# Performance work log

Hardware: AMD Instinct MI355X
Metric: run time of the kernel (lower is better)

The kernel has to match this reference:

```python
import jax, jax.numpy as jnp
import numpy as np

E = 23   # unique experts
K = 3    # active experts per token

def setup_inputs() -> dict:
    key = jax.random.key(0)
    ks = jax.random.split(key, 11)
    d, h, B, N = 1024, 768, 16, 196
    s = 0.02  # init scale so sigmoid gate is non-saturated
    return {
        "x":      jax.random.normal(ks[0], (B, N, d), jnp.float32),
        "gate_w": jax.random.normal(ks[1], (d, E), jnp.float32) * s,
        "gate_b": jnp.zeros((E,), jnp.float32),
        "w1":     jax.random.normal(ks[2], (E, d, h), jnp.float32) * s,
        "b1":     jnp.zeros((E, h), jnp.float32),
        "w2":     jax.random.normal(ks[3], (E, h, d), jnp.float32) * s,
        "b2":     jnp.zeros((E, d), jnp.float32),
        "ws1":    jax.random.normal(ks[4], (d, h), jnp.float32) * s,
        "bs1":    jnp.zeros((h,), jnp.float32),
        "ws2":    jax.random.normal(ks[5], (h, d), jnp.float32) * s,
        "bs2":    jnp.zeros((d,), jnp.float32),
    }

def reference(x, gate_w, gate_b, w1, b1, w2, b2, ws1, bs1, ws2, bs2):
    o_shape = x.shape
    xt = x.reshape(-1, o_shape[-1])            # [T, d]
    T = xt.shape[0]

    # gating: sigmoid gate, top-3 (the 'bias' buffer in the source is zeros)
    gw = jax.nn.sigmoid(xt @ gate_w + gate_b)  # [T, E]
    top_vals, top_idx = jax.lax.top_k(gw, K)   # [T, K]
    tw = top_vals / top_vals.sum(-1, keepdims=True)

    # dense combine weights: tw scattered to [T, E] (0 for unselected experts)
    w_dense = jnp.zeros_like(gw).at[jnp.arange(T)[:, None], top_idx].add(tw)

    # expert MLPs (dense-masked equivalent of the grouped dispatch)
    hh = jax.nn.gelu(jnp.einsum('td,edh->teh', xt, w1) + b1, approximate=False)
    eo = jnp.einsum('teh,ehd->ted', hh, w2) + b2          # [T, E, d]

    # shared expert
    shared = jax.nn.gelu(xt @ ws1 + bs1, approximate=False) @ ws2 + bs2

    out = shared + jnp.einsum('ted,te->td', eo, w_dense)  # [T, d]

    # aux load-balancing loss
    gwn = gw / gw.sum(-1, keepdims=True)
    P = gwn.mean(0)                                       # [E]
    counts = jnp.zeros((E,), gw.dtype).at[top_idx.reshape(-1)].add(1.0)
    Fv = E * counts / (K * T)
    aux = (P * Fv).sum()

    return out.reshape(o_shape), aux
```

## Files before the change

kernel.cpp:

```cpp
#include <hip/hip_runtime.h>
#include <hip/hip_bf16.h>

#define T_TOK 3136
#define DDIM  1024
#define HDIM  768
#define NEXP  23
#define TOPK  3
#define MTILE 128
#define NTILE 128
#define KTILE 32
#define LDSB  40
#define MAXTILES 128
#define MAX_SLOTS 16384
#define GATE_BLOCKS 1568
#define XCVT_BLOCKS 3136

typedef __attribute__((ext_vector_type(8))) short  short8;
typedef __attribute__((ext_vector_type(4))) short  short4v;
typedef __attribute__((ext_vector_type(4))) float  floatx4;

__device__ __forceinline__ short f2b(float f) {
    union { float f; unsigned u; } v; v.f = f;
    unsigned r = v.u + 0x7FFFu + ((v.u >> 16) & 1u);
    return (short)(r >> 16);
}
__device__ __forceinline__ float b2f(short s) {
    union { unsigned u; float f; } v; v.u = ((unsigned)(unsigned short)s) << 16; return v.f;
}
__device__ __forceinline__ float gelu_exact(float v) {
    return 0.5f * v * (1.0f + erff(v * 0.70710678118654752f));
}
__device__ __forceinline__ void gld16(const short* g, short* l) {
    __builtin_amdgcn_global_load_lds(
        (const __attribute__((address_space(1))) void*)g,
        (__attribute__((address_space(3))) void*)l, 16, 0, 0);
}
__device__ __forceinline__ void bar_cnt8() {
    asm volatile("s_waitcnt vmcnt(8) lgkmcnt(0)" ::: "memory");
    __builtin_amdgcn_s_barrier();
    __builtin_amdgcn_sched_barrier(0);
}
__device__ __forceinline__ void bar_cnt0() {
    asm volatile("s_waitcnt vmcnt(0) lgkmcnt(0)" ::: "memory");
    __builtin_amdgcn_s_barrier();
    __builtin_amdgcn_sched_barrier(0);
}

__global__ __launch_bounds__(256) void prep_kernel(
    const float* __restrict__ x, short* __restrict__ xb,
    const float* __restrict__ gw, float* __restrict__ gwT, float* __restrict__ Pf)
{
    __shared__ float tile[32][33];
    if (blockIdx.x < XCVT_BLOCKS) {
        if (blockIdx.x == 0 && threadIdx.x < NEXP) Pf[threadIdx.x] = 0.f;
        int i = blockIdx.x * 256 + threadIdx.x;
        float4 v = ((const float4*)x)[i];
        short4v s = { f2b(v.x), f2b(v.y), f2b(v.z), f2b(v.w) };
        ((short4v*)xb)[i] = s;
        return;
    }
    const int kt = blockIdx.x - XCVT_BLOCKS;
    const int tx = threadIdx.x & 31, ty = threadIdx.x >> 5;
    #pragma unroll
    for (int i = 0; i < 4; i++) {
        int k = ty + i * 8;
        tile[k][tx] = (tx < NEXP) ? gw[(size_t)(kt * 32 + k) * NEXP + tx] : 0.f;
    }
    __syncthreads();
    #pragma unroll
    for (int i = 0; i < 4; i++) {
        int e = ty + i * 8;
        if (e < 24) gwT[(size_t)e * DDIM + kt * 32 + tx] = tile[tx][e];
    }
}

__global__ __launch_bounds__(256) void gate_kernel(
    const float* __restrict__ x, const float* __restrict__ gwT, const float* __restrict__ gb,
    float* __restrict__ Pf, int* __restrict__ top_idx, float* __restrict__ top_w)
{
    const int tid = threadIdx.x;
    const int lane = tid & 63, wave = tid >> 6;
    const int ebase = wave * 6;
    __shared__ float sg[24];
    __shared__ float accP[NEXP];
    if (tid < NEXP) accP[tid] = 0.f;

    for (int t = blockIdx.x; t < T_TOK; t += GATE_BLOCKS) {
        const float4* xr4 = (const float4*)(x + (size_t)t * DDIM);
        float4 xv[4];
        #pragma unroll
        for (int j = 0; j < 4; j++) xv[j] = xr4[j * 64 + lane];

        double a0 = 0, a1 = 0, a2 = 0, a3 = 0, a4 = 0, a5 = 0;
        #pragma unroll
        for (int j = 0; j < 4; j++) {
            const float4* gp = (const float4*)gwT + (size_t)ebase * 256 + j * 64 + lane;
            float4 g0 = gp[0 * 256], g1 = gp[1 * 256], g2 = gp[2 * 256];
            float4 g3 = gp[3 * 256], g4 = gp[4 * 256], g5 = gp[5 * 256];
            float4 xj = xv[j];
            a0 += (double)xj.x * g0.x + (double)xj.y * g0.y + (double)xj.z * g0.z + (double)xj.w * g0.w;
            a1 += (double)xj.x * g1.x + (double)xj.y * g1.y + (double)xj.z * g1.z + (double)xj.w * g1.w;
            a2 += (double)xj.x * g2.x + (double)xj.y * g2.y + (double)xj.z * g2.z + (double)xj.w * g2.w;
            a3 += (double)xj.x * g3.x + (double)xj.y * g3.y + (double)xj.z * g3.z + (double)xj.w * g3.w;
            a4 += (double)xj.x * g4.x + (double)xj.y * g4.y + (double)xj.z * g4.z + (double)xj.w * g4.w;
            a5 += (double)xj.x * g5.x + (double)xj.y * g5.y + (double)xj.z * g5.z + (double)xj.w * g5.w;
        }
        #pragma unroll
        for (int off = 32; off > 0; off >>= 1) {
            a0 += __shfl_xor(a0, off);
            a1 += __shfl_xor(a1, off);
            a2 += __shfl_xor(a2, off);
            a3 += __shfl_xor(a3, off);
            a4 += __shfl_xor(a4, off);
            a5 += __shfl_xor(a5, off);
        }

        if (lane == 0) {
            double av[6] = { a0, a1, a2, a3, a4, a5 };
            #pragma unroll
            for (int i = 0; i < 6; i++) {
                int e = ebase + i;
                if (e < NEXP) {
                    float z = (float)av[i] + gb[e];
                    sg[e] = 1.0f / (1.0f + expf(-z));
                }
            }
        }
        __syncthreads();

        if (tid < NEXP) {
            float s = 0.f;
            #pragma unroll
            for (int e = 0; e < NEXP; e++) s += sg[e];
            accP[tid] += sg[tid] / s;
        }
        if (tid == 0) {
            float v0 = -1.f, v1 = -1.f, v2 = -1.f; int i0 = 0, i1 = 0, i2 = 0;
            for (int e = 0; e < NEXP; e++) {
                float v = sg[e];
                if (v > v0)      { v2 = v1; i2 = i1; v1 = v0; i1 = i0; v0 = v; i0 = e; }
                else if (v > v1) { v2 = v1; i2 = i1; v1 = v; i1 = e; }
                else if (v > v2) { v2 = v; i2 = e; }
            }
            float ts = v0 + v1 + v2;
            top_idx[t * 3 + 0] = i0; top_w[t * 3 + 0] = v0 / ts;
            top_idx[t * 3 + 1] = i1; top_w[t * 3 + 1] = v1 / ts;
            top_idx[t * 3 + 2] = i2; top_w[t * 3 + 2] = v2 / ts;
        }
        __syncthreads();
    }
    if (tid < NEXP) atomicAdd(&Pf[tid], accP[tid]);
}

__global__ __launch_bounds__(1024) void route_kernel(
    const int* __restrict__ top_idx, const float* __restrict__ Pf,
    int* __restrict__ ntl,
    int* __restrict__ slot_t, int* __restrict__ slot_of,
    int* __restrict__ tmap_e, int* __restrict__ tmap_b,
    float* __restrict__ out_aux)
{
    __shared__ int h[NEXP];
    __shared__ int lfill[NEXP];
    __shared__ int soffs[NEXP + 1];
    __shared__ int sntl[NEXP + 1];
    const int tid = threadIdx.x;
    if (tid < NEXP) { h[tid] = 0; lfill[tid] = 0; }
    __syncthreads();
    for (int i = tid; i < T_TOK * 3; i += 1024) atomicAdd(&h[top_idx[i]], 1);
    __syncthreads();
    if (tid == 0) {
        int o = 0, ti = 0;
        for (int e = 0; e < NEXP; e++) {
            int c = h[e];
            int nt = (c + MTILE - 1) / MTILE;
            soffs[e] = o; sntl[e] = nt; ntl[e] = nt;
            for (int j = 0; j < nt; j++) { tmap_e[ti] = e; tmap_b[ti] = o + j * MTILE; ti++; }
            o += nt * MTILE;
        }
        int nts = (T_TOK + MTILE - 1) / MTILE;
        soffs[NEXP] = o; sntl[NEXP] = nts; ntl[NEXP] = nts;
        for (int j = 0; j < nts; j++) { tmap_e[ti] = NEXP; tmap_b[ti] = o + j * MTILE; ti++; }
        ntl[NEXP + 1] = ti;
        float aux = 0.f;
        for (int e = 0; e < NEXP; e++) {
            float P = Pf[e] / (float)T_TOK;
            float F = (float)NEXP * (float)h[e] / (float)(TOPK * T_TOK);
            aux += P * F;
        }
        out_aux[0] = aux;
    }
    __syncthreads();
    for (int e = 0; e <= NEXP; e++) {
        int cnt = (e < NEXP) ? h[e] : T_TOK;
        int s0 = soffs[e] + cnt, s1 = soffs[e] + sntl[e] * MTILE;
        for (int s = s0 + tid; s < s1; s += 1024) slot_t[s] = 0;
    }
    for (int t = tid; t < T_TOK; t += 1024) {
        #pragma unroll
        for (int k = 0; k < TOPK; k++) {
            int e = top_idx[t * 3 + k];
            int pos = atomicAdd(&lfill[e], 1);
            int s = soffs[e] + pos;
            slot_t[s] = t;
            slot_of[t * 4 + k] = s;
        }
        int s = soffs[NEXP] + t;
        slot_t[s] = t;
        slot_of[t * 4 + 3] = s;
    }
}

__global__ __launch_bounds__(256) void gemm1_kernel(
    const short* __restrict__ xb,
    const float* __restrict__ w1, const float* __restrict__ b1,
    const float* __restrict__ ws1, const float* __restrict__ bs1,
    const int* __restrict__ tmap_e, const int* __restrict__ tmap_b,
    const int* __restrict__ ntl,
    const int* __restrict__ slot_t, short* __restrict__ hh)
{
    const int L = blockIdx.x;
    const int xcd = L & 7, sl = L >> 3;
    const int ty = xcd * 16 + sl / 6, tx = sl % 6;
    if (ty >= ntl[NEXP + 1]) return;
    const int e = tmap_e[ty];
    const int slot_base = tmap_b[ty];
    const int n0 = tx * NTILE;
    const float* __restrict__ Wf = (e < NEXP) ? (w1 + (size_t)e * DDIM * HDIM) : ws1;
    const float* __restrict__ Bv = (e < NEXP) ? (b1 + (size_t)e * HDIM) : bs1;

    __shared__ __align__(16) short As[2][MTILE * KTILE];
    __shared__ __align__(16) short Bs[2][NTILE * LDSB];
    __shared__ int toks[MTILE];

    const int tid = threadIdx.x;
    for (int i = tid; i < MTILE; i += 256) toks[i] = slot_t[slot_base + i];

    const int lane = tid & 63, wave = tid >> 6;
    const int mbase = (wave & 1) * 64, nbase = (wave >> 1) * 64;
    const int lc = lane & 15, q = lane >> 4;
    const int xq8 = (q ^ ((lc >> 1) & 3)) << 3;

    const int srow = wave * 16 + (lane >> 2);
    const int c8   = (lane & 3) * 8;

    __syncthreads();
    const short* gA0 = xb + (size_t)toks[srow]      * DDIM + c8;
    const short* gA1 = xb + (size_t)toks[64 + srow] * DDIM + c8;
    const int lofs0 = wave * 512, lofs1 = 2048 + wave * 512;

    const int g = wave, cn = lane;
    const float* gW = Wf + (size_t)(8 * g) * HDIM + n0 + 2 * cn;
    const int bws = (g ^ (cn & 3)) << 3;
    const int bofs0 = (2 * cn) * LDSB + bws, bofs1 = (2 * cn + 1) * LDSB + bws;

    floatx4 acc[4][4];
    #pragma unroll
    for (int m = 0; m < 4; m++)
        #pragma unroll
        for (int n = 0; n < 4; n++) acc[m][n] = (floatx4)0.f;

    const int NT = DDIM / KTILE;
    float2 f[8];
    #pragma unroll
    for (int j = 0; j < 8; j++) f[j] = *(const float2*)(gW + (size_t)j * HDIM);
    gld16(gA0, &As[0][lofs0]);
    gld16(gA1, &As[0][lofs1]);
    __builtin_amdgcn_sched_barrier(0);
    {
        short8 s0, s1;
        #pragma unroll
        for (int j = 0; j < 8; j++) { s0[j] = f2b(f[j].x); s1[j] = f2b(f[j].y); }
        *(short8*)&Bs[0][bofs0] = s0;
        *(short8*)&Bs[0][bofs1] = s1;
    }
    #pragma unroll
    for (int j = 0; j < 8; j++) f[j] = *(const float2*)(gW + (size_t)(KTILE + j) * HDIM);
    bar_cnt8();

    for (int t = 0; t < NT; t++) {
        const int cur = t & 1;
        if (t + 1 < NT) {
            gld16(gA0 + (t + 1) * KTILE, &As[cur ^ 1][lofs0]);
            gld16(gA1 + (t + 1) * KTILE, &As[cur ^ 1][lofs1]);
            __builtin_amdgcn_sched_barrier(0);
            short8 s0, s1;
            #pragma unroll
            for (int j = 0; j < 8; j++) { s0[j] = f2b(f[j].x); s1[j] = f2b(f[j].y); }
            *(short8*)&Bs[cur ^ 1][bofs0] = s0;
            *(short8*)&Bs[cur ^ 1][bofs1] = s1;
        }
        if (t + 2 < NT) {
            #pragma unroll
            for (int j = 0; j < 8; j++)
                f[j] = *(const float2*)(gW + (size_t)((t + 2) * KTILE + j) * HDIM);
        }
        short8 af[4], bf[4];
        #pragma unroll
        for (int m = 0; m < 4; m++) af[m] = *(const short8*)&As[cur][(mbase + m * 16 + lc) * KTILE + q * 8];
        #pragma unroll
        for (int n = 0; n < 4; n++) bf[n] = *(const short8*)&Bs[cur][(nbase + n * 16 + lc) * LDSB + xq8];
        #pragma unroll
        for (int m = 0; m < 4; m++)
            #pragma unroll
            for (int n = 0; n < 4; n++)
                acc[m][n] = __builtin_amdgcn_mfma_f32_16x16x32_bf16(af[m], bf[n], acc[m][n], 0, 0, 0);
        if (t + 1 < NT) {
            if (t + 2 < NT) bar_cnt8();
            else            bar_cnt0();
        }
    }

    #pragma unroll
    for (int n = 0; n < 4; n++) {
        const int col = n0 + nbase + n * 16 + lc;
        const float bb = Bv[col];
        #pragma unroll
        for (int m = 0; m < 4; m++) {
            const int rbase = slot_base + mbase + m * 16 + q * 4;
            #pragma unroll
            for (int r = 0; r < 4; r++) {
                float v = acc[m][n][r] + bb;
                hh[(size_t)(rbase + r) * HDIM + col] = f2b(gelu_exact(v));
            }
        }
    }
}

__global__ __launch_bounds__(256) void gemm2_kernel(
    const short* __restrict__ hh,
    const float* __restrict__ w2, const float* __restrict__ b2,
    const float* __restrict__ ws2, const float* __restrict__ bs2,
    const int* __restrict__ tmap_e, const int* __restrict__ tmap_b,
    const int* __restrict__ ntl,
    short* __restrict__ eo)
{
    const int L = blockIdx.x;
    const int xcd = L & 7, sl = L >> 3;
    const int ty = xcd * 16 + sl / 8, tx = sl & 7;
    if (ty >= ntl[NEXP + 1]) return;
    const int e = tmap_e[ty];
    const int slot_base = tmap_b[ty];
    const int n0 = tx * NTILE;
    const float* __restrict__ Wf = (e < NEXP) ? (w2 + (size_t)e * HDIM * DDIM) : ws2;
    const float* __restrict__ Bv = (e < NEXP) ? (b2 + (size_t)e * DDIM) : bs2;

    __shared__ __align__(16) short As[2][MTILE * KTILE];
    __shared__ __align__(16) short Bs[2][NTILE * LDSB];

    const int tid = threadIdx.x;
    const int lane = tid & 63, wave = tid >> 6;
    const int mbase = (wave & 1) * 64, nbase = (wave >> 1) * 64;
    const int lc = lane & 15, q = lane >> 4;
    const int xq8 = (q ^ ((lc >> 1) & 3)) << 3;

    const int srow = wave * 16 + (lane >> 2);
    const int c8   = (lane & 3) * 8;

    const short* gA0 = hh + (size_t)(slot_base + srow)      * HDIM + c8;
    const short* gA1 = hh + (size_t)(slot_base + 64 + srow) * HDIM + c8;
    const int lofs0 = wave * 512, lofs1 = 2048 + wave * 512;

    const int g = wave, cn = lane;
    const float* gW = Wf + (size_t)(8 * g) * DDIM + n0 + 2 * cn;
    const int bws = (g ^ (cn & 3)) << 3;
    const int bofs0 = (2 * cn) * LDSB + bws, bofs1 = (2 * cn + 1) * LDSB + bws;

    floatx4 acc[4][4];
    #pragma unroll
    for (int m = 0; m < 4; m++)
        #pragma unroll
        for (int n = 0; n < 4; n++) acc[m][n] = (floatx4)0.f;

    const int NT = HDIM / KTILE;
    float2 f[8];
    #pragma unroll
    for (int j = 0; j < 8; j++) f[j] = *(const float2*)(gW + (size_t)j * DDIM);
    gld16(gA0, &As[0][lofs0]);
    gld16(gA1, &As[0][lofs1]);
    __builtin_amdgcn_sched_barrier(0);
    {
        short8 s0, s1;
        #pragma unroll
        for (int j = 0; j < 8; j++) { s0[j] = f2b(f[j].x); s1[j] = f2b(f[j].y); }
        *(short8*)&Bs[0][bofs0] = s0;
        *(short8*)&Bs[0][bofs1] = s1;
    }
    #pragma unroll
    for (int j = 0; j < 8; j++) f[j] = *(const float2*)(gW + (size_t)(KTILE + j) * DDIM);
    bar_cnt8();

    for (int t = 0; t < NT; t++) {
        const int cur = t & 1;
        if (t + 1 < NT) {
            gld16(gA0 + (t + 1) * KTILE, &As[cur ^ 1][lofs0]);
            gld16(gA1 + (t + 1) * KTILE, &As[cur ^ 1][lofs1]);
            __builtin_amdgcn_sched_barrier(0);
            short8 s0, s1;
            #pragma unroll
            for (int j = 0; j < 8; j++) { s0[j] = f2b(f[j].x); s1[j] = f2b(f[j].y); }
            *(short8*)&Bs[cur ^ 1][bofs0] = s0;
            *(short8*)&Bs[cur ^ 1][bofs1] = s1;
        }
        if (t + 2 < NT) {
            #pragma unroll
            for (int j = 0; j < 8; j++)
                f[j] = *(const float2*)(gW + (size_t)((t + 2) * KTILE + j) * DDIM);
        }
        short8 af[4], bf[4];
        #pragma unroll
        for (int m = 0; m < 4; m++) af[m] = *(const short8*)&As[cur][(mbase + m * 16 + lc) * KTILE + q * 8];
        #pragma unroll
        for (int n = 0; n < 4; n++) bf[n] = *(const short8*)&Bs[cur][(nbase + n * 16 + lc) * LDSB + xq8];
        #pragma unroll
        for (int m = 0; m < 4; m++)
            #pragma unroll
            for (int n = 0; n < 4; n++)
                acc[m][n] = __builtin_amdgcn_mfma_f32_16x16x32_bf16(af[m], bf[n], acc[m][n], 0, 0, 0);
        if (t + 1 < NT) {
            if (t + 2 < NT) bar_cnt8();
            else            bar_cnt0();
        }
    }

    #pragma unroll
    for (int n = 0; n < 4; n++) {
        const int col = n0 + nbase + n * 16 + lc;
        const float bb = Bv[col];
        #pragma unroll
        for (int m = 0; m < 4; m++) {
            const int rbase = slot_base + mbase + m * 16 + q * 4;
            #pragma unroll
            for (int r = 0; r < 4; r++)
                eo[(size_t)(rbase + r) * DDIM + col] = f2b(acc[m][n][r] + bb);
        }
    }
}

__global__ __launch_bounds__(256) void combine_kernel(
    const short* __restrict__ eo, const float* __restrict__ top_w,
    const int* __restrict__ slot_of, float* __restrict__ out)
{
    const int t = blockIdx.x;
    const int c = threadIdx.x * 4;
    const int s0 = slot_of[t * 4 + 0], s1 = slot_of[t * 4 + 1];
    const int s2 = slot_of[t * 4 + 2], s3 = slot_of[t * 4 + 3];
    const float w0 = top_w[t * 3 + 0], w1 = top_w[t * 3 + 1], w2 = top_w[t * 3 + 2];
    short4v a = *(const short4v*)(eo + (size_t)s0 * DDIM + c);
    short4v b = *(const short4v*)(eo + (size_t)s1 * DDIM + c);
    short4v d = *(const short4v*)(eo + (size_t)s2 * DDIM + c);
    short4v s = *(const short4v*)(eo + (size_t)s3 * DDIM + c);
    float4 o;
    o.x = b2f(s.x) + w0 * b2f(a.x) + w1 * b2f(b.x) + w2 * b2f(d.x);
    o.y = b2f(s.y) + w0 * b2f(a.y) + w1 * b2f(b.y) + w2 * b2f(d.y);
    o.z = b2f(s.z) + w0 * b2f(a.z) + w1 * b2f(b.z) + w2 * b2f(d.z);
    o.w = b2f(s.w) + w0 * b2f(a.w) + w1 * b2f(b.w) + w2 * b2f(d.w);
    *(float4*)(out + (size_t)t * DDIM + c) = o;
}

extern "C" void kernel_launch(void* const* d_in, const int* in_sizes, int n_in,
                              void* d_out, int out_size, void* d_ws, size_t ws_size,
                              hipStream_t stream)
{
    const float* x   = (const float*)d_in[0];
    const float* gw  = (const float*)d_in[1];
    const float* gb  = (const float*)d_in[2];
    const float* w1  = (const float*)d_in[3];
    const float* b1  = (const float*)d_in[4];
    const float* w2  = (const float*)d_in[5];
    const float* b2  = (const float*)d_in[6];
    const float* ws1 = (const float*)d_in[7];
    const float* bs1 = (const float*)d_in[8];
    const float* ws2 = (const float*)d_in[9];
    const float* bs2 = (const float*)d_in[10];
    float* out = (float*)d_out;

    char* p = (char*)d_ws;
    auto alloc = [&](size_t bytes) -> char* {
        char* r = p; p += (bytes + 255) & ~(size_t)255; return r;
    };
    int*   top_idx  = (int*)  alloc((size_t)T_TOK * 3 * 4);
    float* top_w    = (float*)alloc((size_t)T_TOK * 3 * 4);
    float* Pf       = (float*)alloc(NEXP * 4);
    int*   ntl      = (int*)  alloc((NEXP + 2) * 4);
    int*   slot_t   = (int*)  alloc((size_t)MAX_SLOTS * 4);
    int*   slot_of  = (int*)  alloc((size_t)T_TOK * 4 * 4);
    int*   tmap_e   = (int*)  alloc((size_t)MAXTILES * 4);
    int*   tmap_b   = (int*)  alloc((size_t)MAXTILES * 4);
    float* gwT      = (float*)alloc((size_t)24 * DDIM * 4);
    short* xb       = (short*)alloc((size_t)T_TOK * DDIM * 2);
    short* hh       = (short*)alloc((size_t)MAX_SLOTS * HDIM * 2);
    short* eo       = (short*)alloc((size_t)MAX_SLOTS * DDIM * 2);

    prep_kernel<<<XCVT_BLOCKS + DDIM / 32, 256, 0, stream>>>(x, xb, gw, gwT, Pf);
    gate_kernel<<<GATE_BLOCKS, 256, 0, stream>>>(x, gwT, gb, Pf, top_idx, top_w);
    route_kernel<<<1, 1024, 0, stream>>>(top_idx, Pf, ntl, slot_t, slot_of,
                                         tmap_e, tmap_b, out + (size_t)T_TOK * DDIM);
    gemm1_kernel<<<8 * 16 * 6, 256, 0, stream>>>(
        xb, w1, b1, ws1, bs1, tmap_e, tmap_b, ntl, slot_t, hh);
    gemm2_kernel<<<8 * 16 * 8, 256, 0, stream>>>(
        hh, w2, b2, ws2, bs2, tmap_e, tmap_b, ntl, eo);
    combine_kernel<<<T_TOK, 256, 0, stream>>>(eo, top_w, slot_of, out);
}
```

Before: 380.0 us.

## Use 8 waves per block in expert GEMMs with 64x32 per-wave tiles

Doubles the threads per block in both grouped GEMM kernels from 256 to 512. Each wave now computes a 64x32 output sub-tile instead of 64x64, and the A and B tile loads are split across 8 waves, so each thread issues half as many loads and conversions. The aim is more waves per CU to hide the global load and fp32-to-bf16 conversion latency. The cost is lower MFMA work per LDS fragment read, and the higher register use allowed under launch_bounds 512 may limit occupancy.

```diff
diff --git a/kernel.cpp b/kernel.cpp
--- a/kernel.cpp
+++ b/kernel.cpp
@@ -35,8 +35,8 @@
         (const __attribute__((address_space(1))) void*)g,
         (__attribute__((address_space(3))) void*)l, 16, 0, 0);
 }
-__device__ __forceinline__ void bar_cnt8() {
-    asm volatile("s_waitcnt vmcnt(8) lgkmcnt(0)" ::: "memory");
+__device__ __forceinline__ void bar_cnt4() {
+    asm volatile("s_waitcnt vmcnt(4) lgkmcnt(0)" ::: "memory");
     __builtin_amdgcn_s_barrier();
     __builtin_amdgcn_sched_barrier(0);
 }
@@ -210,7 +210,7 @@
     }
 }
 
-__global__ __launch_bounds__(256) void gemm1_kernel(
+__global__ __launch_bounds__(512) void gemm1_kernel(
     const short* __restrict__ xb,
     const float* __restrict__ w1, const float* __restrict__ b1,
     const float* __restrict__ ws1, const float* __restrict__ bs1,
@@ -233,10 +233,10 @@
     __shared__ int toks[MTILE];
 
     const int tid = threadIdx.x;
-    for (int i = tid; i < MTILE; i += 256) toks[i] = slot_t[slot_base + i];
+    for (int i = tid; i < MTILE; i += 512) toks[i] = slot_t[slot_base + i];
 
     const int lane = tid & 63, wave = tid >> 6;
-    const int mbase = (wave & 1) * 64, nbase = (wave >> 1) * 64;
+    const int mbase = (wave & 1) * 64, nbase = (wave >> 1) * 32;
     const int lc = lane & 15, q = lane >> 4;
     const int xq8 = (q ^ ((lc >> 1) & 3)) << 3;
 
@@ -244,74 +244,71 @@
     const int c8   = (lane & 3) * 8;
 
     __syncthreads();
-    const short* gA0 = xb + (size_t)toks[srow]      * DDIM + c8;
-    const short* gA1 = xb + (size_t)toks[64 + srow] * DDIM + c8;
-    const int lofs0 = wave * 512, lofs1 = 2048 + wave * 512;
-
-    const int g = wave, cn = lane;
-    const float* gW = Wf + (size_t)(8 * g) * HDIM + n0 + 2 * cn;
-    const int bws = (g ^ (cn & 3)) << 3;
+    const short* gA = xb + (size_t)toks[srow] * DDIM + c8;
+    const int lofs = wave * 512;
+
+    const int cn = lane;
+    const float* gW = Wf + (size_t)(4 * wave) * HDIM + n0 + 2 * cn;
+    const int bws = ((((wave >> 1) ^ (cn & 3)) << 3) + (wave & 1) * 4);
     const int bofs0 = (2 * cn) * LDSB + bws, bofs1 = (2 * cn + 1) * LDSB + bws;
 
-    floatx4 acc[4][4];
+    floatx4 acc[4][2];
     #pragma unroll
     for (int m = 0; m < 4; m++)
         #pragma unroll
-        for (int n = 0; n < 4; n++) acc[m][n] = (floatx4)0.f;
+        for (int n = 0; n < 2; n++) acc[m][n] = (floatx4)0.f;
 
     const int NT = DDIM / KTILE;
-    float2 f[8];
-    #pragma unroll
-    for (int j = 0; j < 8; j++) f[j] = *(const float2*)(gW + (size_t)j * HDIM);
-    gld16(gA0, &As[0][lofs0]);
-    gld16(gA1, &As[0][lofs1]);
+    float2 f[4];
+    #pragma unroll
+    for (int j = 0; j < 4; j++) f[j] = *(const float2*)(gW + (size_t)j * HDIM);
+    gld16(gA, &As[0][lofs]);
     __builtin_amdgcn_sched_barrier(0);
     {
-        short8 s0, s1;
-        #pragma unroll
-        for (int j = 0; j < 8; j++) { s0[j] = f2b(f[j].x); s1[j] = f2b(f[j].y); }
-        *(short8*)&Bs[0][bofs0] = s0;
-        *(short8*)&Bs[0][bofs1] = s1;
-    }
-    #pragma unroll
-    for (int j = 0; j < 8; j++) f[j] = *(const float2*)(gW + (size_t)(KTILE + j) * HDIM);
-    bar_cnt8();
+        short4v s0, s1;
+        #pragma unroll
+        for (int j = 0; j < 4; j++) { s0[j] = f2b(f[j].x); s1[j] = f2b(f[j].y); }
+        *(short4v*)&Bs[0][bofs0] = s0;
+        *(short4v*)&Bs[0][bofs1] = s1;
+    }
+    #pragma unroll
+    for (int j = 0; j < 4; j++) f[j] = *(const float2*)(gW + (size_t)(KTILE + j) * HDIM);
+    bar_cnt4();
 
     for (int t = 0; t < NT; t++) {
         const int cur = t & 1;
         if (t + 1 < NT) {
-            gld16(gA0 + (t + 1) * KTILE, &As[cur ^ 1][lofs0]);
-            gld16(gA1 + (t + 1) * KTILE, &As[cur ^ 1][lofs1]);
+            gld16(gA + (t + 1) * KTILE, &As[cur ^ 1][lofs]);
             __builtin_amdgcn_sched_barrier(0);
-            short8 s0, s1;
-            #pragma unroll
-            for (int j = 0; j < 8; j++) { s0[j] = f2b(f[j].x); s1[j] = f2b(f[j].y); }
-            *(short8*)&Bs[cur ^ 1][bofs0] = s0;
-            *(short8*)&Bs[cur ^ 1][bofs1] = s1;
+            short4v s0, s1;
+            #pragma unroll
+            for (int j = 0; j < 4; j++) { s0[j] = f2b(f[j].x); s1[j] = f2b(f[j].y); }
+            *(short4v*)&Bs[cur ^ 1][bofs0] = s0;
+            *(short4v*)&Bs[cur ^ 1][bofs1] = s1;
         }
         if (t + 2 < NT) {
             #pragma unroll
-            for (int j = 0; j < 8; j++)
+            for (int j = 0; j < 4; j++)
                 f[j] = *(const float2*)(gW + (size_t)((t + 2) * KTILE + j) * HDIM);
         }
-        short8 af[4], bf[4];
+        short8 af[4], bf[2];
         #pragma unroll
         for (int m = 0; m < 4; m++) af[m] = *(const short8*)&As[cur][(mbase + m * 16 + lc) * KTILE + q * 8];
         #pragma unroll
-        for (int n = 0; n < 4; n++) bf[n] = *(const short8*)&Bs[cur][(nbase + n * 16 + lc) * LDSB + xq8];
+        for (int n = 0; n < 2; n++) bf[n] = *(const short8*)&Bs[cur][(nbase + n * 16 + lc) * LDSB + xq8];
         #pragma unroll
         for (int m = 0; m < 4; m++)
             #pragma unroll
-            for (int n = 0; n < 4; n++)
+            for (int n = 0; n < 2; n++)
                 acc[m][n] = __builtin_amdgcn_mfma_f32_16x16x32_bf16(af[m], bf[n], acc[m][n], 0, 0, 0);
         if (t + 1 < NT) {
-            if (t + 2 < NT) bar_cnt8();
+            if (t + 2 < NT) bar_cnt4();
             else            bar_cnt0();
         }
     }
 
     #pragma unroll
-    for (int n = 0; n < 4; n++) {
+    for (int n = 0; n < 2; n++) {
         const int col = n0 + nbase + n * 16 + lc;
         const float bb = Bv[col];
         #pragma unroll
@@ -326,7 +323,7 @@
     }
 }
 
-__global__ __launch_bounds__(256) void gemm2_kernel(
+__global__ __launch_bounds__(512) void gemm2_kernel(
     const short* __restrict__ hh,
     const float* __restrict__ w2, const float* __restrict__ b2,
     const float* __restrict__ ws2, const float* __restrict__ bs2,
@@ -349,81 +346,78 @@
 
     const int tid = threadIdx.x;
     const int lane = tid & 63, wave = tid >> 6;
-    const int mbase = (wave & 1) * 64, nbase = (wave >> 1) * 64;
+    const int mbase = (wave & 1) * 64, nbase = (wave >> 1) * 32;
     const int lc = lane & 15, q = lane >> 4;
     const int xq8 = (q ^ ((lc >> 1) & 3)) << 3;
 
     const int srow = wave * 16 + (lane >> 2);
     const int c8   = (lane & 3) * 8;
 
-    const short* gA0 = hh + (size_t)(slot_base + srow)      * HDIM + c8;
-    const short* gA1 = hh + (size_t)(slot_base + 64 + srow) * HDIM + c8;
-    const int lofs0 = wave * 512, lofs1 = 2048 + wave * 512;
-
-    const int g = wave, cn = lane;
-    const float* gW = Wf + (size_t)(8 * g) * DDIM + n0 + 2 * cn;
-    const int bws = (g ^ (cn & 3)) << 3;
+    const short* gA = hh + (size_t)(slot_base + srow) * HDIM + c8;
+    const int lofs = wave * 512;
+
+    const int cn = lane;
+    const float* gW = Wf + (size_t)(4 * wave) * DDIM + n0 + 2 * cn;
+    const int bws = ((((wave >> 1) ^ (cn & 3)) << 3) + (wave & 1) * 4);
     const int bofs0 = (2 * cn) * LDSB + bws, bofs1 = (2 * cn + 1) * LDSB + bws;
 
-    floatx4 acc[4][4];
+    floatx4 acc[4][2];
     #pragma unroll
     for (int m = 0; m < 4; m++)
         #pragma unroll
-        for (int n = 0; n < 4; n++) acc[m][n] = (floatx4)0.f;
+        for (int n = 0; n < 2; n++) acc[m][n] = (floatx4)0.f;
 
     const int NT = HDIM / KTILE;
-    float2 f[8];
-    #pragma unroll
-    for (int j = 0; j < 8; j++) f[j] = *(const float2*)(gW + (size_t)j * DDIM);
-    gld16(gA0, &As[0][lofs0]);
-    gld16(gA1, &As[0][lofs1]);
+    float2 f[4];
+    #pragma unroll
+    for (int j = 0; j < 4; j++) f[j] = *(const float2*)(gW + (size_t)j * DDIM);
+    gld16(gA, &As[0][lofs]);
     __builtin_amdgcn_sched_barrier(0);
     {
-        short8 s0, s1;
-        #pragma unroll
-        for (int j = 0; j < 8; j++) { s0[j] = f2b(f[j].x); s1[j] = f2b(f[j].y); }
-        *(short8*)&Bs[0][bofs0] = s0;
-        *(short8*)&Bs[0][bofs1] = s1;
-    }
-    #pragma unroll
-    for (int j = 0; j < 8; j++) f[j] = *(const float2*)(gW + (size_t)(KTILE + j) * DDIM);
-    bar_cnt8();
+        short4v s0, s1;
+        #pragma unroll
+        for (int j = 0; j < 4; j++) { s0[j] = f2b(f[j].x); s1[j] = f2b(f[j].y); }
+        *(short4v*)&Bs[0][bofs0] = s0;
+        *(short4v*)&Bs[0][bofs1] = s1;
+    }
+    #pragma unroll
+    for (int j = 0; j < 4; j++) f[j] = *(const float2*)(gW + (size_t)(KTILE + j) * DDIM);
+    bar_cnt4();
 
     for (int t = 0; t < NT; t++) {
         const int cur = t & 1;
         if (t + 1 < NT) {
-            gld16(gA0 + (t + 1) * KTILE, &As[cur ^ 1][lofs0]);
-            gld16(gA1 + (t + 1) * KTILE, &As[cur ^ 1][lofs1]);
+            gld16(gA + (t + 1) * KTILE, &As[cur ^ 1][lofs]);
             __builtin_amdgcn_sched_barrier(0);
-            short8 s0, s1;
-            #pragma unroll
-            for (int j = 0; j < 8; j++) { s0[j] = f2b(f[j].x); s1[j] = f2b(f[j].y); }
-            *(short8*)&Bs[cur ^ 1][bofs0] = s0;
-            *(short8*)&Bs[cur ^ 1][bofs1] = s1;
+            short4v s0, s1;
+            #pragma unroll
+            for (int j = 0; j < 4; j++) { s0[j] = f2b(f[j].x); s1[j] = f2b(f[j].y); }
+            *(short4v*)&Bs[cur ^ 1][bofs0] = s0;
+            *(short4v*)&Bs[cur ^ 1][bofs1] = s1;
         }
         if (t + 2 < NT) {
             #pragma unroll
-            for (int j = 0; j < 8; j++)
+            for (int j = 0; j < 4; j++)
                 f[j] = *(const float2*)(gW + (size_t)((t + 2) * KTILE + j) * DDIM);
         }
-        short8 af[4], bf[4];
+        short8 af[4], bf[2];
         #pragma unroll
         for (int m = 0; m < 4; m++) af[m] = *(const short8*)&As[cur][(mbase + m * 16 + lc) * KTILE + q * 8];
         #pragma unroll
-        for (int n = 0; n < 4; n++) bf[n] = *(const short8*)&Bs[cur][(nbase + n * 16 + lc) * LDSB + xq8];
+        for (int n = 0; n < 2; n++) bf[n] = *(const short8*)&Bs[cur][(nbase + n * 16 + lc) * LDSB + xq8];
         #pragma unroll
         for (int m = 0; m < 4; m++)
             #pragma unroll
-            for (int n = 0; n < 4; n++)
+            for (int n = 0; n < 2; n++)
                 acc[m][n] = __builtin_amdgcn_mfma_f32_16x16x32_bf16(af[m], bf[n], acc[m][n], 0, 0, 0);
         if (t + 1 < NT) {
-            if (t + 2 < NT) bar_cnt8();
+            if (t + 2 < NT) bar_cnt4();
             else            bar_cnt0();
         }
     }
 
     #pragma unroll
-    for (int n = 0; n < 4; n++) {
+    for (int n = 0; n < 2; n++) {
         const int col = n0 + nbase + n * 16 + lc;
         const float bb = Bv[col];
         #pragma unroll
@@ -495,9 +489,9 @@
     gate_kernel<<<GATE_BLOCKS, 256, 0, stream>>>(x, gwT, gb, Pf, top_idx, top_w);
     route_kernel<<<1, 1024, 0, stream>>>(top_idx, Pf, ntl, slot_t, slot_of,
                                          tmap_e, tmap_b, out + (size_t)T_TOK * DDIM);
-    gemm1_kernel<<<8 * 16 * 6, 256, 0, stream>>>(
+    gemm1_kernel<<<8 * 16 * 6, 512, 0, stream>>>(
         xb, w1, b1, ws1, bs1, tmap_e, tmap_b, ntl, slot_t, hh);
-    gemm2_kernel<<<8 * 16 * 8, 256, 0, stream>>>(
+    gemm2_kernel<<<8 * 16 * 8, 512, 0, stream>>>(
         hh, w2, b2, ws2, bs2, tmap_e, tmap_b, ntl, eo);
     combine_kernel<<<T_TOK, 256, 0, stream>>>(eo, top_w, slot_of, out);
 }
```

New measurement: 376.5 us. About the same (-0.9%).
